# Performance work log

Hardware: AMD Instinct MI355X
Metric: run time of the kernel (lower is better)

## Reference

```python
import math
import jax, jax.numpy as jnp
import numpy as np

K = 7  # kernel_size
PAD = 3  # padding (kernel_size//2)


def _base_kernels():
    # 4 oriented anisotropic Gaussian kernels, [4, K, K]
    sigma1, sigma2 = 2.5, 1.0
    ax = jnp.linspace(-(K // 2), K // 2, K)
    xx, yy = jnp.meshgrid(ax, ax, indexing='ij')
    ks = []
    for theta in (0.0, math.pi / 4, math.pi / 2, 3 * math.pi / 4):
        c, s = math.cos(theta), math.sin(theta)
        x_rot = xx * c + yy * s
        y_rot = -xx * s + yy * c
        k = jnp.exp(-(x_rot ** 2 / (2 * sigma1 ** 2) + y_rot ** 2 / (2 * sigma2 ** 2)))
        ks.append(k / k.sum())
    return jnp.stack(ks, axis=0)


def setup_inputs() -> dict:
    key = jax.random.key(0)
    ks = jax.random.split(key, 8)
    B, C, H, W, mid = 2, 256, 256, 256, 16
    x = jax.random.normal(ks[0], (B, C, H, W), dtype=jnp.float32)
    angle_map = jax.random.uniform(ks[1], (B, H, W), dtype=jnp.float32) * math.pi
    reduce_w = jax.random.normal(ks[2], (mid, C), dtype=jnp.float32) * (1.0 / math.sqrt(C))
    expand_w = jax.random.normal(ks[3], (C, mid), dtype=jnp.float32) * (1.0 / math.sqrt(mid))
    w1 = jax.random.normal(ks[4], (8, 2), dtype=jnp.float32) * (1.0 / math.sqrt(2))
    b1 = jnp.zeros((8,), dtype=jnp.float32)
    w2 = jax.random.normal(ks[5], (4, 8), dtype=jnp.float32) * (1.0 / math.sqrt(8))
    b2 = jnp.zeros((4,), dtype=jnp.float32)
    return {"x": x, "angle_map": angle_map, "reduce_w": reduce_w,
            "expand_w": expand_w, "w1": w1, "b1": b1, "w2": w2, "b2": b2}


def reference(x, angle_map, reduce_w, expand_w, w1, b1, w2, b2):
    B, C, H, W = x.shape
    mid = reduce_w.shape[0]
    base = _base_kernels()  # [4,K,K], constant buffer

    # 1x1 reduce conv
    x_low = jnp.einsum('bchw,mc->bmhw', x, reduce_w)  # [B,mid,H,W]

    # per-pixel mixing weights from angle: MLP(2->8->4) + softmax
    angle_feat = jnp.stack([jnp.sin(2 * angle_map), jnp.cos(2 * angle_map)], axis=-1)  # [B,H,W,2]
    h = jax.nn.relu(jnp.einsum('bhwi,oi->bhwo', angle_feat, w1) + b1)
    weights = jax.nn.softmax(jnp.einsum('bhwi,oi->bhwo', h, w2) + b2, axis=-1)  # [B,H,W,4]

    # reflect pad, then cross-correlate each channel with the 4 base kernels.
    # Equivalent to the original unfold+einsum: out = sum_k w_k * (x_low * base_k)
    x_pad = jnp.pad(x_low, ((0, 0), (0, 0), (PAD, PAD), (PAD, PAD)), mode='reflect')
    Hp, Wp = x_pad.shape[-2:]
    y = jax.lax.conv_general_dilated(
        x_pad.reshape(B * mid, 1, Hp, Wp), base[:, None],  # [4,1,K,K]
        window_strides=(1, 1), padding='VALID')  # [B*mid,4,H,W]
    y = y.reshape(B, mid, 4, H, W)

    out_low = jnp.einsum('bmkhw,bhwk->bmhw', y, weights)  # [B,mid,H,W]
    out = jnp.einsum('bmhw,cm->bchw', out_low, expand_w)  # 1x1 expand conv
    return out
```

## Files before the change

### kernel.cpp

```cpp
#include <hip/hip_runtime.h>

#define H_   256
#define W_   256
#define HW_  65536
#define C_   256
#define MID  16
#define B_   2

__global__ __launch_bounds__(256) void k0_prep(const float* __restrict__ rw,
                                               float* __restrict__ base_out,
                                               float* __restrict__ rwt) {
    __shared__ float s_k[4][49];
    __shared__ float s_inv[4];
    int t = threadIdx.x;
    if (t < 196) {
        int k = t / 49, p = t % 49;
        int i = p / 7, j = p % 7;
        float xx = (float)(i - 3), yy = (float)(j - 3);
        const float cs[4] = {1.0f, 0.70710678118654752f, 0.0f, -0.70710678118654752f};
        const float sn[4] = {0.0f, 0.70710678118654752f, 1.0f, 0.70710678118654752f};
        float c = cs[k], s = sn[k];
        float xr = xx * c + yy * s;
        float yr = -xx * s + yy * c;
        float v = expf(-(xr * xr * 0.08f + yr * yr * 0.5f));
        s_k[k][p] = v;
    }
    __syncthreads();
    if (t < 4) {
        float s = 0.f;
        for (int p = 0; p < 49; ++p) s += s_k[t][p];
        s_inv[t] = 1.0f / s;
    }
    __syncthreads();
    if (t < 196) base_out[t] = s_k[t / 49][t % 49] * s_inv[t / 49];
    for (int idx = t; idx < MID * C_; idx += 256) {
        int c = idx >> 4, m = idx & 15;
        rwt[idx] = rw[m * C_ + c];
    }
}

__global__ __launch_bounds__(256) void kA_reduce(const float* __restrict__ x,
                                                 const float* __restrict__ rwt,
                                                 float* __restrict__ xlow) {
    int bh = blockIdx.x;
    int b = bh >> 8, h = bh & 255;
    int w = threadIdx.x;
    const float* xp = x + (size_t)b * C_ * HW_ + h * W_ + w;
    float acc[MID];
#pragma unroll
    for (int m = 0; m < MID; ++m) acc[m] = 0.f;
    for (int cb = 0; cb < C_; cb += 16) {
        float xv[16];
#pragma unroll
        for (int i = 0; i < 16; ++i)
            xv[i] = __builtin_nontemporal_load(xp + (size_t)(cb + i) * HW_);
#pragma unroll
        for (int i = 0; i < 16; ++i) {
#pragma unroll
            for (int m = 0; m < MID; ++m)
                acc[m] = fmaf(rwt[(cb + i) * MID + m], xv[i], acc[m]);
        }
    }
    float4* op = (float4*)(xlow + ((size_t)b * HW_ + h * W_ + w) * MID);
    op[0] = make_float4(acc[0], acc[1], acc[2], acc[3]);
    op[1] = make_float4(acc[4], acc[5], acc[6], acc[7]);
    op[2] = make_float4(acc[8], acc[9], acc[10], acc[11]);
    op[3] = make_float4(acc[12], acc[13], acc[14], acc[15]);
}

__global__ __launch_bounds__(256) void kB_conv(const float* __restrict__ xlow,
                                               const float* __restrict__ base,
                                               const float* __restrict__ angle,
                                               const float* __restrict__ w1,
                                               const float* __restrict__ b1,
                                               const float* __restrict__ w2,
                                               const float* __restrict__ b2,
                                               float* __restrict__ olow) {
    int bid = blockIdx.x;
    int mh = bid & 1;
    int h = (bid >> 1) & 255;
    int b = bid >> 9;
    int w = threadIdx.x;

    float a2 = 2.0f * angle[(size_t)b * HW_ + h * W_ + w];
    float f0 = __sinf(a2), f1 = __cosf(a2);
    float hb[8];
#pragma unroll
    for (int j = 0; j < 8; ++j)
        hb[j] = fmaxf(fmaf(w1[j * 2], f0, fmaf(w1[j * 2 + 1], f1, b1[j])), 0.f);
    float lg[4];
#pragma unroll
    for (int k = 0; k < 4; ++k) {
        float s = b2[k];
#pragma unroll
        for (int j = 0; j < 8; ++j) s = fmaf(w2[k * 8 + j], hb[j], s);
        lg[k] = s;
    }
    float mx = fmaxf(fmaxf(lg[0], lg[1]), fmaxf(lg[2], lg[3]));
    float wk[4];
    float ssum = 0.f;
#pragma unroll
    for (int k = 0; k < 4; ++k) { wk[k] = __expf(lg[k] - mx); ssum += wk[k]; }
    float inv = 1.0f / ssum;
#pragma unroll
    for (int k = 0; k < 4; ++k) wk[k] *= inv;

    int cc[7];
#pragma unroll
    for (int dx = 0; dx < 7; ++dx) {
        int c0 = w + dx - 3;
        cc[dx] = c0 < 0 ? -c0 : (c0 > 255 ? 510 - c0 : c0);
    }
    float acc[8];
#pragma unroll
    for (int m = 0; m < 8; ++m) acc[m] = 0.f;
    const float* xb = xlow + (size_t)b * HW_ * MID + mh * 8;
    for (int dy = 0; dy < 7; ++dy) {
        int hy = h + dy - 3;
        hy = hy < 0 ? -hy : (hy > 255 ? 510 - hy : hy);
        float e[7];
#pragma unroll
        for (int dx = 0; dx < 7; ++dx) {
            int tp = dy * 7 + dx;
            e[dx] = fmaf(wk[0], base[tp],
                    fmaf(wk[1], base[49 + tp],
                    fmaf(wk[2], base[98 + tp], wk[3] * base[147 + tp])));
        }
        const float* rowb = xb + (size_t)hy * W_ * MID;
#pragma unroll
        for (int dx = 0; dx < 7; ++dx) {
            const float4* p = (const float4*)(rowb + cc[dx] * MID);
            float4 v0 = p[0];
            float4 v1 = p[1];
            float ed = e[dx];
            acc[0] = fmaf(ed, v0.x, acc[0]);
            acc[1] = fmaf(ed, v0.y, acc[1]);
            acc[2] = fmaf(ed, v0.z, acc[2]);
            acc[3] = fmaf(ed, v0.w, acc[3]);
            acc[4] = fmaf(ed, v1.x, acc[4]);
            acc[5] = fmaf(ed, v1.y, acc[5]);
            acc[6] = fmaf(ed, v1.z, acc[6]);
            acc[7] = fmaf(ed, v1.w, acc[7]);
        }
    }
    float4* op = (float4*)(olow + ((size_t)b * HW_ + h * W_ + w) * MID + mh * 8);
    op[0] = make_float4(acc[0], acc[1], acc[2], acc[3]);
    op[1] = make_float4(acc[4], acc[5], acc[6], acc[7]);
}

__global__ __launch_bounds__(256) void kC_expand(const float* __restrict__ olow,
                                                 const float* __restrict__ ew,
                                                 float* __restrict__ out) {
    int bid = blockIdx.x;
    int cch = bid & 7;
    int h = (bid >> 3) & 255;
    int b = bid >> 11;
    int w = threadIdx.x;
    const float4* ip = (const float4*)(olow + ((size_t)b * HW_ + h * W_ + w) * MID);
    float4 m0 = ip[0], m1 = ip[1], m2 = ip[2], m3 = ip[3];
    float* ob = out + ((size_t)b * C_ + cch * 32) * HW_ + h * W_ + w;
#pragma unroll 8
    for (int ci = 0; ci < 32; ++ci) {
        const float* wc = ew + (size_t)(cch * 32 + ci) * MID;
        float s;
        s = wc[0] * m0.x;
        s = fmaf(wc[1], m0.y, s);
        s = fmaf(wc[2], m0.z, s);
        s = fmaf(wc[3], m0.w, s);
        s = fmaf(wc[4], m1.x, s);
        s = fmaf(wc[5], m1.y, s);
        s = fmaf(wc[6], m1.z, s);
        s = fmaf(wc[7], m1.w, s);
        s = fmaf(wc[8], m2.x, s);
        s = fmaf(wc[9], m2.y, s);
        s = fmaf(wc[10], m2.z, s);
        s = fmaf(wc[11], m2.w, s);
        s = fmaf(wc[12], m3.x, s);
        s = fmaf(wc[13], m3.y, s);
        s = fmaf(wc[14], m3.z, s);
        s = fmaf(wc[15], m3.w, s);
        __builtin_nontemporal_store(s, ob + (size_t)ci * HW_);
    }
}

extern "C" void kernel_launch(void* const* d_in, const int* in_sizes, int n_in,
                              void* d_out, int out_size, void* d_ws, size_t ws_size,
                              hipStream_t stream) {
    const float* x     = (const float*)d_in[0];
    const float* angle = (const float*)d_in[1];
    const float* rw    = (const float*)d_in[2];
    const float* ew    = (const float*)d_in[3];
    const float* w1    = (const float*)d_in[4];
    const float* b1    = (const float*)d_in[5];
    const float* w2    = (const float*)d_in[6];
    const float* b2    = (const float*)d_in[7];
    float* out = (float*)d_out;

    float* wsf  = (float*)d_ws;
    float* base = wsf;
    float* rwt  = wsf + 256;
    float* xlow = wsf + 8192;
    float* olow = wsf + 8192 + B_ * HW_ * MID;

    hipLaunchKernelGGL(k0_prep,   dim3(1),    dim3(256), 0, stream, rw, base, rwt);
    hipLaunchKernelGGL(kA_reduce, dim3(512),  dim3(256), 0, stream, x, rwt, xlow);
    hipLaunchKernelGGL(kB_conv,   dim3(1024), dim3(256), 0, stream,
                       xlow, base, angle, w1, b1, w2, b2, olow);
    hipLaunchKernelGGL(kC_expand, dim3(4096), dim3(256), 0, stream, olow, ew, out);
}
```

Measured before the change: 295.8 us.

## Switch xlow to planar layout, precompute conv taps, drop weight transpose, retile expand

```diff
diff --git a/kernel.cpp b/kernel.cpp
--- a/kernel.cpp
+++ b/kernel.cpp
@@ -7,9 +7,7 @@
 #define MID  16
 #define B_   2
 
-__global__ __launch_bounds__(256) void k0_prep(const float* __restrict__ rw,
-                                               float* __restrict__ base_out,
-                                               float* __restrict__ rwt) {
+__global__ __launch_bounds__(256) void k0_prep(float* __restrict__ base_out) {
     __shared__ float s_k[4][49];
     __shared__ float s_inv[4];
     int t = threadIdx.x;
@@ -33,15 +31,11 @@
     }
     __syncthreads();
     if (t < 196) base_out[t] = s_k[t / 49][t % 49] * s_inv[t / 49];
-    for (int idx = t; idx < MID * C_; idx += 256) {
-        int c = idx >> 4, m = idx & 15;
-        rwt[idx] = rw[m * C_ + c];
-    }
-}
-
-__global__ __launch_bounds__(256) void kA_reduce(const float* __restrict__ x,
-                                                 const float* __restrict__ rwt,
-                                                 float* __restrict__ xlow) {
+}
+
+__global__ __launch_bounds__(256, 2) void kA_reduce(const float* __restrict__ x,
+                                                    const float* __restrict__ rw,
+                                                    float* __restrict__ xlow) {
     int bh = blockIdx.x;
     int b = bh >> 8, h = bh & 255;
     int w = threadIdx.x;
@@ -53,29 +47,27 @@
         float xv[16];
 #pragma unroll
         for (int i = 0; i < 16; ++i)
-            xv[i] = __builtin_nontemporal_load(xp + (size_t)(cb + i) * HW_);
+            xv[i] = xp[(size_t)(cb + i) * HW_];
 #pragma unroll
         for (int i = 0; i < 16; ++i) {
 #pragma unroll
             for (int m = 0; m < MID; ++m)
-                acc[m] = fmaf(rwt[(cb + i) * MID + m], xv[i], acc[m]);
+                acc[m] = fmaf(rw[m * C_ + cb + i], xv[i], acc[m]);
         }
     }
-    float4* op = (float4*)(xlow + ((size_t)b * HW_ + h * W_ + w) * MID);
-    op[0] = make_float4(acc[0], acc[1], acc[2], acc[3]);
-    op[1] = make_float4(acc[4], acc[5], acc[6], acc[7]);
-    op[2] = make_float4(acc[8], acc[9], acc[10], acc[11]);
-    op[3] = make_float4(acc[12], acc[13], acc[14], acc[15]);
-}
-
-__global__ __launch_bounds__(256) void kB_conv(const float* __restrict__ xlow,
-                                               const float* __restrict__ base,
-                                               const float* __restrict__ angle,
-                                               const float* __restrict__ w1,
-                                               const float* __restrict__ b1,
-                                               const float* __restrict__ w2,
-                                               const float* __restrict__ b2,
-                                               float* __restrict__ olow) {
+    float* op = xlow + (size_t)b * MID * HW_ + h * W_ + w;
+#pragma unroll
+    for (int m = 0; m < MID; ++m) op[(size_t)m * HW_] = acc[m];
+}
+
+__global__ __launch_bounds__(256, 4) void kB_conv(const float* __restrict__ xlow,
+                                                  const float* __restrict__ base,
+                                                  const float* __restrict__ angle,
+                                                  const float* __restrict__ w1,
+                                                  const float* __restrict__ b1,
+                                                  const float* __restrict__ w2,
+                                                  const float* __restrict__ b2,
+                                                  float* __restrict__ olow) {
     int bid = blockIdx.x;
     int mh = bid & 1;
     int h = (bid >> 1) & 255;
@@ -105,44 +97,42 @@
 #pragma unroll
     for (int k = 0; k < 4; ++k) wk[k] *= inv;
 
+    float e[49];
+#pragma unroll
+    for (int tp = 0; tp < 49; ++tp)
+        e[tp] = fmaf(wk[0], base[tp],
+                fmaf(wk[1], base[49 + tp],
+                fmaf(wk[2], base[98 + tp], wk[3] * base[147 + tp])));
+
     int cc[7];
 #pragma unroll
     for (int dx = 0; dx < 7; ++dx) {
         int c0 = w + dx - 3;
         cc[dx] = c0 < 0 ? -c0 : (c0 > 255 ? 510 - c0 : c0);
     }
-    float acc[8];
-#pragma unroll
-    for (int m = 0; m < 8; ++m) acc[m] = 0.f;
-    const float* xb = xlow + (size_t)b * HW_ * MID + mh * 8;
+    int rr[7];
+#pragma unroll
     for (int dy = 0; dy < 7; ++dy) {
         int hy = h + dy - 3;
-        hy = hy < 0 ? -hy : (hy > 255 ? 510 - hy : hy);
-        float e[7];
-#pragma unroll
-        for (int dx = 0; dx < 7; ++dx) {
-            int tp = dy * 7 + dx;
-            e[dx] = fmaf(wk[0], base[tp],
-                    fmaf(wk[1], base[49 + tp],
-                    fmaf(wk[2], base[98 + tp], wk[3] * base[147 + tp])));
+        rr[dy] = (hy < 0 ? -hy : (hy > 255 ? 510 - hy : hy)) * W_;
+    }
+
+    const float* xb = xlow + (size_t)b * MID * HW_ + (size_t)mh * 8 * HW_;
+    float acc[8];
+#pragma unroll
+    for (int m = 0; m < 8; ++m) {
+        const float* pm = xb + (size_t)m * HW_;
+        float s = 0.f;
+#pragma unroll
+        for (int dy = 0; dy < 7; ++dy) {
+            const float* r = pm + rr[dy];
+#pragma unroll
+            for (int dx = 0; dx < 7; ++dx)
+                s = fmaf(e[dy * 7 + dx], r[cc[dx]], s);
         }
-        const float* rowb = xb + (size_t)hy * W_ * MID;
-#pragma unroll
-        for (int dx = 0; dx < 7; ++dx) {
-            const float4* p = (const float4*)(rowb + cc[dx] * MID);
-            float4 v0 = p[0];
-            float4 v1 = p[1];
-            float ed = e[dx];
-            acc[0] = fmaf(ed, v0.x, acc[0]);
-            acc[1] = fmaf(ed, v0.y, acc[1]);
-            acc[2] = fmaf(ed, v0.z, acc[2]);
-            acc[3] = fmaf(ed, v0.w, acc[3]);
-            acc[4] = fmaf(ed, v1.x, acc[4]);
-            acc[5] = fmaf(ed, v1.y, acc[5]);
-            acc[6] = fmaf(ed, v1.z, acc[6]);
-            acc[7] = fmaf(ed, v1.w, acc[7]);
-        }
-    }
+        acc[m] = s;
+    }
+
     float4* op = (float4*)(olow + ((size_t)b * HW_ + h * W_ + w) * MID + mh * 8);
     op[0] = make_float4(acc[0], acc[1], acc[2], acc[3]);
     op[1] = make_float4(acc[4], acc[5], acc[6], acc[7]);
@@ -152,16 +142,17 @@
                                                  const float* __restrict__ ew,
                                                  float* __restrict__ out) {
     int bid = blockIdx.x;
-    int cch = bid & 7;
-    int h = (bid >> 3) & 255;
-    int b = bid >> 11;
+    int cq = bid & 3;
+    int h = (bid >> 2) & 255;
+    int b = bid >> 10;
     int w = threadIdx.x;
     const float4* ip = (const float4*)(olow + ((size_t)b * HW_ + h * W_ + w) * MID);
     float4 m0 = ip[0], m1 = ip[1], m2 = ip[2], m3 = ip[3];
-    float* ob = out + ((size_t)b * C_ + cch * 32) * HW_ + h * W_ + w;
+    float* ob = out + ((size_t)b * C_ + cq * 64) * HW_ + h * W_ + w;
+    const float* wb = ew + (size_t)cq * 64 * MID;
 #pragma unroll 8
-    for (int ci = 0; ci < 32; ++ci) {
-        const float* wc = ew + (size_t)(cch * 32 + ci) * MID;
+    for (int ci = 0; ci < 64; ++ci) {
+        const float* wc = wb + ci * MID;
         float s;
         s = wc[0] * m0.x;
         s = fmaf(wc[1], m0.y, s);
@@ -198,13 +189,12 @@
 
     float* wsf  = (float*)d_ws;
     float* base = wsf;
-    float* rwt  = wsf + 256;
-    float* xlow = wsf + 8192;
-    float* olow = wsf + 8192 + B_ * HW_ * MID;
-
-    hipLaunchKernelGGL(k0_prep,   dim3(1),    dim3(256), 0, stream, rw, base, rwt);
-    hipLaunchKernelGGL(kA_reduce, dim3(512),  dim3(256), 0, stream, x, rwt, xlow);
+    float* xlow = wsf + 256;
+    float* olow = xlow + (size_t)B_ * MID * HW_;
+
+    hipLaunchKernelGGL(k0_prep,   dim3(1),    dim3(256), 0, stream, base);
+    hipLaunchKernelGGL(kA_reduce, dim3(512),  dim3(256), 0, stream, x, rw, xlow);
     hipLaunchKernelGGL(kB_conv,   dim3(1024), dim3(256), 0, stream,
                        xlow, base, angle, w1, b1, w2, b2, olow);
-    hipLaunchKernelGGL(kC_expand, dim3(4096), dim3(256), 0, stream, olow, ew, out);
-}
+    hipLaunchKernelGGL(kC_expand, dim3(2048), dim3(256), 0, stream, olow, ew, out);
+}
```

Measured after the change: 336.4 us. 13.7% more time.
